# Kernel tuning notes

Hardware: AMD Instinct MI355X
Metric: run time of the kernel (lower is better)

## Reference

```python
import jax, jax.numpy as jnp
import numpy as np

B, L, DM, H = 16, 2048, 1024, 16
DK = DM // H
FACTOR = 1


def setup_inputs() -> dict:
    key = jax.random.key(0)
    ks = jax.random.split(key, 8)
    s = 0.02
    return {
        "queries": jax.random.normal(ks[0], (B, L, DM), jnp.float32),
        "keys": jax.random.normal(ks[1], (B, L, DM), jnp.float32),
        "values": jax.random.normal(ks[2], (B, L, DM), jnp.float32),
        "Wq": jax.random.normal(ks[3], (DM, DM), jnp.float32) * s,
        "Wk": jax.random.normal(ks[4], (DM, DM), jnp.float32) * s,
        "Wv": jax.random.normal(ks[5], (DM, DM), jnp.float32) * s,
        "Wo": jax.random.normal(ks[6], (DM, DM), jnp.float32) * s,
        "bo": jnp.zeros((DM,), jnp.float32),
    }


def reference(queries, keys, values, Wq, Wk, Wv, Wo, bo):
    # Projections (torch Linear: y = x @ W.T), then [B, H, DK, L] layout
    Q = (queries @ Wq.T).reshape(B, L, H, DK).transpose(0, 2, 3, 1)
    K = (keys @ Wk.T).reshape(B, L, H, DK).transpose(0, 2, 3, 1)
    V = (values @ Wv.T).reshape(B, L, H, DK).transpose(0, 2, 3, 1)

    # FFT cross-correlation along time
    qf = jnp.fft.rfft(Q, axis=-1)
    kf = jnp.fft.rfft(K, axis=-1)
    corr = jnp.fft.irfft(qf * jnp.conj(kf), n=L, axis=-1)  # [B, H, DK, L]

    # time_delay_agg_inference (eval path); B == H so torch's right-aligned
    # broadcast maps the batch axis of delay/weights onto the HEAD axis.
    top_k = int(FACTOR * np.log(L))
    mean_value = jnp.mean(corr, axis=1)                     # [B, DK, L]
    weights, delay = jax.lax.top_k(mean_value, top_k)       # [B, DK, K]
    w = jax.nn.softmax(weights, axis=-1)

    pos = jnp.arange(L)
    agg = jnp.zeros_like(V)
    for i in range(top_k):  # small fixed loop (top_k = 7)
        idx = (pos[None, None, :] + delay[:, :, i][:, :, None]) % L  # first axis aligns with H
        pattern = jnp.take_along_axis(V, jnp.broadcast_to(idx[None], V.shape), axis=-1)
        agg = agg + pattern * w[:, :, i][None, :, :, None]

    out = agg.transpose(0, 3, 1, 2).reshape(B, L, DM)  # [B, L, H*DK]
    out = out @ Wo.T + bo
    return out, corr
```

## Files before the change

kernel.cpp:

```cpp
#include <hip/hip_runtime.h>
#include <hip/hip_fp16.h>
#include <hip/hip_bf16.h>
#include <cstdint>
#include <cstddef>

typedef float  f32x4 __attribute__((ext_vector_type(4)));
typedef short  s16x8 __attribute__((ext_vector_type(8)));
typedef unsigned short u16;
typedef unsigned int   u32;
typedef u32 u32x4 __attribute__((ext_vector_type(4)));
typedef u32 u32x2 __attribute__((ext_vector_type(2)));

#define TOPK 7

__device__ __forceinline__ u32 bfpk(float re, float im) {
  __hip_bfloat162 h = __float22bfloat162_rn(make_float2(re, im));
  return *(u32*)&h;
}
__device__ __forceinline__ u16 f2bf(float f) {
  __hip_bfloat16 h = __float2bfloat16(f);
  return *(u16*)&h;
}
__device__ __forceinline__ float b2f(u16 s) {
  return __uint_as_float(((u32)s) << 16);
}
__device__ __forceinline__ float2 bfup(u32 p) {
  float2 r; r.x = b2f((u16)(p & 0xffffu)); r.y = b2f((u16)(p >> 16)); return r;
}
__device__ __forceinline__ u32 pkf16(float c, float s) {
  __half2 h = __floats2half2_rn(c, s);
  return *(u32*)&h;
}
__device__ __forceinline__ float2 upf16(u32 p) {
  __half2 h; *(u32*)&h = p;
  float2 r; r.x = __low2float(h); r.y = __high2float(h); return r;
}

typedef __attribute__((address_space(1))) void gvoid;
typedef __attribute__((address_space(3))) void lvoid;
__device__ __forceinline__ void gl_lds16(const void* g, void* l) {
  __builtin_amdgcn_global_load_lds((gvoid*)g, (lvoid*)l, 16, 0, 0);
}

__global__ void cvt_kernel(const float* __restrict__ src, u16* __restrict__ dst, int n8) {
  int i = blockIdx.x * 256 + threadIdx.x;
  if (i >= n8) return;
  const f32x4* sp = (const f32x4*)src + (size_t)i * 2;
  f32x4 a = sp[0], b = sp[1];
  u32x4 o;
  o[0] = bfpk(a[0], a[1]); o[1] = bfpk(a[2], a[3]);
  o[2] = bfpk(b[0], b[1]); o[3] = bfpk(b[2], b[3]);
  *(u32x4*)(dst + (size_t)i * 8) = o;
}

template<int MODE>
__global__ __launch_bounds__(256, 2) void gemm_bt(
    const void* __restrict__ Aptr, const u16* __restrict__ Bw,
    void* __restrict__ Cout, const float* __restrict__ bias)
{
  constexpr int K = 1024, N = 1024;
  __shared__ __align__(16) u16 lA[128 * 32];
  __shared__ __align__(16) u16 lB[128 * 32];

  int bx = blockIdx.x;
  int wg = (bx & 7) * 256 + (bx >> 3);
  int tm = wg >> 3, tn = wg & 7;
  int m0 = tm * 128, n0 = tn * 128;

  int t = threadIdx.x;
  int wid = t >> 6, lane = t & 63;
  int wm = wid >> 1, wn = wid & 1;
  int lr = lane & 15, kb = lane >> 4;

  f32x4 acc[4][4] = {};

  for (int kt = 0; kt < 32; ++kt) {
    int k0 = kt * 32;
    if constexpr (MODE == 0) {
      const float* A = (const float*)Aptr;
      int r = t >> 1, half = t & 1;
      const float* ap = A + (size_t)(m0 + r) * K + k0 + half * 16;
      f32x4 v[4];
#pragma unroll
      for (int g = 0; g < 4; ++g) v[g] = ((const f32x4*)ap)[g];
      u32x4 o0, o1;
      o0[0] = bfpk(v[0][0], v[0][1]); o0[1] = bfpk(v[0][2], v[0][3]);
      o0[2] = bfpk(v[1][0], v[1][1]); o0[3] = bfpk(v[1][2], v[1][3]);
      o1[0] = bfpk(v[2][0], v[2][1]); o1[1] = bfpk(v[2][2], v[2][3]);
      o1[2] = bfpk(v[3][0], v[3][1]); o1[3] = bfpk(v[3][2], v[3][3]);
      *(u32x4*)&lA[r * 32 + half * 16]     = o0;
      *(u32x4*)&lA[r * 32 + half * 16 + 8] = o1;
    } else {
      const u16* A = (const u16*)Aptr;
#pragma unroll
      for (int it = 0; it < 2; ++it) {
        int o = t * 16 + it * 4096;
        int e = o >> 1;
        int row = e >> 5, col = e & 31;
        gl_lds16(A + (size_t)(m0 + row) * K + k0 + col,
                 (char*)lA + wid * 1024 + it * 4096);
      }
    }
#pragma unroll
    for (int it = 0; it < 2; ++it) {
      int o = t * 16 + it * 4096;
      int e = o >> 1;
      int row = e >> 5, col = e & 31;
      gl_lds16(Bw + (size_t)(n0 + row) * K + k0 + col,
               (char*)lB + wid * 1024 + it * 4096);
    }
    __syncthreads();

    s16x8 af[4], bf[4];
#pragma unroll
    for (int mi = 0; mi < 4; ++mi)
      af[mi] = *(const s16x8*)&lA[(wm * 64 + mi * 16 + lr) * 32 + kb * 8];
#pragma unroll
    for (int ni = 0; ni < 4; ++ni)
      bf[ni] = *(const s16x8*)&lB[(wn * 64 + ni * 16 + lr) * 32 + kb * 8];
#pragma unroll
    for (int mi = 0; mi < 4; ++mi)
#pragma unroll
      for (int ni = 0; ni < 4; ++ni)
        acc[mi][ni] = __builtin_amdgcn_mfma_f32_16x16x32_bf16(af[mi], bf[ni], acc[mi][ni], 0, 0, 0);
    __syncthreads();
  }

#pragma unroll
  for (int mi = 0; mi < 4; ++mi) {
    int mbase = m0 + wm * 64 + mi * 16 + kb * 4;
#pragma unroll
    for (int ni = 0; ni < 4; ++ni) {
      int nn = n0 + wn * 64 + ni * 16 + lr;
      if constexpr (MODE == 0) {
        u16* OT = (u16*)Cout;
        int b = mbase >> 11, l = mbase & 2047;
        u32x2 pk;
        pk[0] = bfpk(acc[mi][ni][0], acc[mi][ni][1]);
        pk[1] = bfpk(acc[mi][ni][2], acc[mi][ni][3]);
        *(u32x2*)(OT + ((size_t)((b << 10) + nn)) * 2048 + l) = pk;
      } else {
        float* C = (float*)Cout;
        float bv = bias[nn];
#pragma unroll
        for (int j = 0; j < 4; ++j)
          C[(size_t)(mbase + j) * N + nn] = acc[mi][ni][j] + bv;
      }
    }
  }
}


__device__ __constant__ const int BRv[32] = {
  0,16,8,24,4,20,12,28,2,18,10,26,6,22,14,30,
  1,17,9,25,5,21,13,29,3,19,11,27,7,23,15,31};
__device__ const float C32v[16] = {
  1.0f, 0.98078528f, 0.92387953f, 0.83146961f,
  0.70710678f, 0.55557023f, 0.38268343f, 0.19509032f,
  0.0f, -0.19509032f, -0.38268343f, -0.55557023f,
  -0.70710678f, -0.83146961f, -0.92387953f, -0.98078528f};
__device__ const float S32v[16] = {
  0.0f, 0.19509032f, 0.38268343f, 0.55557023f,
  0.70710678f, 0.83146961f, 0.92387953f, 0.98078528f,
  1.0f, 0.98078528f, 0.92387953f, 0.83146961f,
  0.70710678f, 0.55557023f, 0.38268343f, 0.19509032f};

#define TWIDX(j) ((j) + ((j) >> 4))

template<bool INV>
__device__ __forceinline__ void dft32(float* xr, float* xi) {
#pragma unroll
  for (int s = 0; s < 5; ++s) {
    const int half = 1 << s, step = 16 >> s;
#pragma unroll
    for (int blk = 0; blk < 32; blk += 2 * half) {
#pragma unroll
      for (int j = 0; j < half; ++j) {
        float wr = C32v[j * step];
        float wi = INV ? S32v[j * step] : -S32v[j * step];
        int p = blk + j, q = p + half;
        float vr = xr[q] * wr - xi[q] * wi;
        float vi = xr[q] * wi + xi[q] * wr;
        xr[q] = xr[p] - vr; xi[q] = xi[p] - vi;
        xr[p] = xr[p] + vr; xi[p] = xi[p] + vi;
      }
    }
  }
}

__device__ __forceinline__ void fft_fwd_row(const u32* __restrict__ zrow, int tt,
                                            u32* wsr, const u32* twp,
                                            float* xr, float* xi) {
#pragma unroll
  for (int i = 0; i < 32; ++i) {
    float2 v = bfup(zrow[32 * BRv[i] + tt]);
    xr[i] = v.x; xi[i] = v.y;
  }
  dft32<false>(xr, xi);
#pragma unroll
  for (int k1 = 0; k1 < 32; ++k1) {
    float2 w = upf16(twp[TWIDX(tt * k1)]);
    wsr[k1 * 33 + tt] = bfpk(xr[k1] * w.x - xi[k1] * w.y,
                             xr[k1] * w.y + xi[k1] * w.x);
  }
  __syncthreads();
#pragma unroll
  for (int i = 0; i < 32; ++i) {
    float2 v = bfup(wsr[tt * 33 + BRv[i]]);
    xr[i] = v.x; xi[i] = v.y;
  }
  __syncthreads();
  dft32<false>(xr, xi);
}

__device__ __forceinline__ void spec_bin(
    float zlQr, float zlQi, float zpQr, float zpQi,
    float zlKr, float zlKi, float zpKr, float zpKi,
    float wr, float wi, float& outr, float& outi)
{
  float aQr = zlQr + zpQr, aQi = zlQi - zpQi;
  float bQr = zlQr - zpQr, bQi = zlQi + zpQi;
  float gQr  = aQr + wr * bQi + wi * bQr;
  float gQi  = aQi - (wr * bQr - wi * bQi);
  float gQpr = aQr - wr * bQi - wi * bQr;
  float gQpi = -aQi - wr * bQr + wi * bQi;
  float aKr = zlKr + zpKr, aKi = zlKi - zpKi;
  float bKr = zlKr - zpKr, bKi = zlKi + zpKi;
  float gKr  = aKr + wr * bKi + wi * bKr;
  float gKi  = aKi - (wr * bKr - wi * bKi);
  float gKpr = aKr - wr * bKi - wi * bKr;
  float gKpi = -aKi - wr * bKr + wi * bKi;
  float ctr = gQr * gKr + gQi * gKi;
  float cti = gQi * gKr - gQr * gKi;
  float cpr = gQpr * gKpr + gQpi * gKpi;
  float cpi = gQpi * gKpr - gQpr * gKpi;
  float utr = ctr + cpr, uti = cti - cpi;
  float vtr = ctr - cpr, vti = cti + cpi;
  outr = (utr - wr * vti + wi * vtr) * (1.0f / 8192.0f);
  outi = (uti + wr * vtr + wi * vti) * (1.0f / 8192.0f);
}

__global__ __launch_bounds__(256) void fftcorr_kernel(
    const u16* __restrict__ Qt, const u16* __restrict__ Kt, float* __restrict__ corr)
{
  __shared__ u32 twp[1088];
  __shared__ u32 wsb[8][1056];

  int t = threadIdx.x;
#pragma unroll
  for (int i = 0; i < 4; ++i) {
    int j = t + 256 * i;
    float s, c;
    __sincosf((float)j * -6.135923151e-3f, &s, &c);
    twp[TWIDX(j)] = pkf16(c, s);
  }
  __syncthreads();

  int rl = t >> 5, tt = t & 31;
  int row = blockIdx.x * 8 + rl;
  const u32* qrow = (const u32*)Qt + (size_t)row * 1024;
  const u32* krow = (const u32*)Kt + (size_t)row * 1024;
  u32* wsr = wsb[rl];
  int lw = t & 63;
  int paddr = (((-tt) & 31) | (lw & 32)) << 2;
  bool f0 = (tt == 0);

  float xr[32], xi[32];
  u32 zkp[32], ap[32], zcp[32];

  fft_fwd_row(krow, tt, wsr, twp, xr, xi);
#pragma unroll
  for (int i = 0; i < 32; ++i) zkp[i] = bfpk(xr[i], xi[i]);
  fft_fwd_row(qrow, tt, wsr, twp, xr, xi);
#pragma unroll
  for (int i = 0; i < 32; ++i) ap[i] = bfpk(xr[i], xi[i]);

#pragma unroll
  for (int j = 0; j < 16; ++j) {
    u32 qpA = (u32)__builtin_amdgcn_ds_bpermute(paddr, (int)ap[31 - j]);
    u32 kpA = (u32)__builtin_amdgcn_ds_bpermute(paddr, (int)zkp[31 - j]);
    u32 qpB = (u32)__builtin_amdgcn_ds_bpermute(paddr, (int)ap[j]);
    u32 kpB = (u32)__builtin_amdgcn_ds_bpermute(paddr, (int)zkp[j]);
    if (f0) {
      qpA = ap[(32 - j) & 31];  kpA = zkp[(32 - j) & 31];
      qpB = ap[(j + 1) & 31];   kpB = zkp[(j + 1) & 31];
    }
    float2 bA = upf16(twp[TWIDX((tt >> 1) + 16 * j)]);
    float2 bB = upf16(twp[TWIDX((tt >> 1) + 16 * (31 - j))]);
    bool oddk = (tt & 1);
    float mr = oddk ? 0.999995293810f : 1.0f;
    float mi = oddk ? -3.067956763e-3f : 0.0f;
    float wAr = bA.x * mr - bA.y * mi, wAi = bA.x * mi + bA.y * mr;
    float wBr = bB.x * mr - bB.y * mi, wBi = bB.x * mi + bB.y * mr;
    float2 zl, zp, kl, kp;
    float or_, oi_;
    zl = bfup(ap[j]);      zp = bfup(qpA);
    kl = bfup(zkp[j]);     kp = bfup(kpA);
    spec_bin(zl.x, zl.y, zp.x, zp.y, kl.x, kl.y, kp.x, kp.y, wAr, wAi, or_, oi_);
    zcp[j] = bfpk(or_, oi_);
    zl = bfup(ap[31 - j]); zp = bfup(qpB);
    kl = bfup(zkp[31 - j]); kp = bfup(kpB);
    spec_bin(zl.x, zl.y, zp.x, zp.y, kl.x, kl.y, kp.x, kp.y, wBr, wBi, or_, oi_);
    zcp[31 - j] = bfpk(or_, oi_);
  }

#define SWPU(a, b) { u32 tp = zcp[a]; zcp[a] = zcp[b]; zcp[b] = tp; }
  SWPU(1, 16) SWPU(2, 8) SWPU(3, 24) SWPU(5, 20) SWPU(6, 12) SWPU(7, 28)
  SWPU(9, 18) SWPU(11, 26) SWPU(13, 22) SWPU(15, 30) SWPU(19, 25) SWPU(23, 29)
#undef SWPU
#pragma unroll
  for (int i = 0; i < 32; ++i) {
    float2 v = bfup(zcp[i]);
    xr[i] = v.x; xi[i] = v.y;
  }
  dft32<true>(xr, xi);
#pragma unroll
  for (int v1 = 0; v1 < 32; ++v1) {
    float2 w = upf16(twp[TWIDX(tt * v1)]);
    wsr[v1 * 33 + tt] = bfpk(xr[v1] * w.x + xi[v1] * w.y,
                             xi[v1] * w.x - xr[v1] * w.y);
  }
  __syncthreads();
#pragma unroll
  for (int i = 0; i < 32; ++i) {
    float2 v = bfup(wsr[tt * 33 + BRv[i]]);
    xr[i] = v.x; xi[i] = v.y;
  }
  dft32<true>(xr, xi);

  float2* crow = (float2*)(corr + (size_t)row * 2048);
#pragma unroll
  for (int v2 = 0; v2 < 32; ++v2) {
    float2 o; o.x = xr[v2]; o.y = xi[v2];
    crow[tt + 32 * v2] = o;
  }
}

__global__ void mean_kernel(const float* __restrict__ corr, float* __restrict__ meanp) {
  int idx = blockIdx.x * 256 + threadIdx.x;
  int l4 = idx & 511;
  int d  = (idx >> 9) & 63;
  int b  = idx >> 15;
  const f32x4* cp = (const f32x4*)corr;
  f32x4 s = {};
#pragma unroll
  for (int h = 0; h < 16; ++h)
    s += cp[((size_t)(b * 1024 + h * 64 + d)) * 512 + l4];
  ((f32x4*)meanp)[(size_t)(b * 64 + d) * 512 + l4] = s * 0.0625f;
}

__global__ __launch_bounds__(256) void topk_kernel(
    const float* __restrict__ meanp, int* __restrict__ delays, float* __restrict__ wts)
{
  int row = blockIdx.x;
  const float* mr = meanp + (size_t)row * 2048;
  int t = threadIdx.x;
  float v[8];
#pragma unroll
  for (int j = 0; j < 8; ++j) v[j] = mr[t * 8 + j];
  __shared__ float sV[256];
  __shared__ int   sI[256];
  __shared__ float topv[TOPK];
  __shared__ int   topi[TOPK];
  for (int rnd = 0; rnd < TOPK; ++rnd) {
    float bv = v[0]; int bi = t * 8;
#pragma unroll
    for (int j = 1; j < 8; ++j)
      if (v[j] > bv) { bv = v[j]; bi = t * 8 + j; }
    sV[t] = bv; sI[t] = bi;
    __syncthreads();
    for (int off = 128; off > 0; off >>= 1) {
      if (t < off) {
        float ov = sV[t + off]; int oi = sI[t + off];
        if (ov > sV[t] || (ov == sV[t] && oi < sI[t])) { sV[t] = ov; sI[t] = oi; }
      }
      __syncthreads();
    }
    int wi = sI[0];
    if (t == 0) { topv[rnd] = sV[0]; topi[rnd] = wi; }
    if ((wi >> 3) == t) {
#pragma unroll
      for (int j = 0; j < 8; ++j)
        if ((wi & 7) == j) v[j] = -__builtin_inff();
    }
    __syncthreads();
  }
  if (t == 0) {
    float mx = topv[0], sum = 0.f, e[TOPK];
#pragma unroll
    for (int i = 0; i < TOPK; ++i) { e[i] = expf(topv[i] - mx); sum += e[i]; }
#pragma unroll
    for (int i = 0; i < TOPK; ++i) {
      wts[row * 8 + i]    = e[i] / sum;
      delays[row * 8 + i] = topi[i];
    }
  }
}

__global__ __launch_bounds__(256) void agg_kernel(
    const u16* __restrict__ Vt, const float* __restrict__ wts,
    const int* __restrict__ delays, u16* __restrict__ aggt)
{
  int row = blockIdx.x;
  int c = row & 1023;
  __shared__ __align__(16) float Vs[4608];
  __shared__ float wsh[TOPK];
  __shared__ int   dsh[TOPK];
  int t = threadIdx.x;
  if (t < TOPK) { wsh[t] = wts[c * 8 + t]; dsh[t] = delays[c * 8 + t]; }
  const u16* vr = Vt + (size_t)row * 2048;
  u32x4 rv = *(const u32x4*)(vr + t * 8);
  alignas(16) u16 uv[8];
  *(u32x4*)uv = rv;
  int f0 = t * 8;
#pragma unroll
  for (int j = 0; j < 8; ++j) {
    float fv = b2f(uv[j]);
    int f  = f0 + j;
    int f2 = f + 2048;
    Vs[f  + ((f  >> 5) << 2)] = fv;
    Vs[f2 + ((f2 >> 5) << 2)] = fv;
  }
  __syncthreads();
  float o[8] = {0, 0, 0, 0, 0, 0, 0, 0};
#pragma unroll
  for (int i = 0; i < TOPK; ++i) {
    float w = wsh[i]; int dl = dsh[i];
    int base = f0 + dl;
#pragma unroll
    for (int j = 0; j < 8; ++j) {
      int f = base + j;
      o[j] += w * Vs[f + ((f >> 5) << 2)];
    }
  }
  u32x4 ob;
  ob[0] = bfpk(o[0], o[1]); ob[1] = bfpk(o[2], o[3]);
  ob[2] = bfpk(o[4], o[5]); ob[3] = bfpk(o[6], o[7]);
  *(u32x4*)(aggt + (size_t)row * 2048 + f0) = ob;
}

__global__ __launch_bounds__(256) void transpose_kernel(
    const u16* __restrict__ aggt, u16* __restrict__ aggb)
{
  int bid = blockIdx.x;
  int lt = bid & 31;
  int ct = (bid >> 5) & 15;
  int b  = bid >> 9;
  __shared__ __align__(16) u16 tile[64][72];
  int t = threadIdx.x;
  int r = t >> 2, seg = t & 3;
  const u16* src = aggt + ((size_t)(b * 1024 + ct * 64 + r)) * 2048 + lt * 64 + seg * 16;
  u32x4 v0 = *(const u32x4*)src;
  u32x4 v1 = *(const u32x4*)(src + 8);
  *(u32x4*)&tile[r][seg * 16]     = v0;
  *(u32x4*)&tile[r][seg * 16 + 8] = v1;
  __syncthreads();
  alignas(16) u16 tmp[16];
#pragma unroll
  for (int j = 0; j < 16; ++j) tmp[j] = tile[seg * 16 + j][r];
  u16* dst = aggb + ((size_t)(b * 2048 + lt * 64 + r)) * 1024 + ct * 64 + seg * 16;
  *(u32x4*)dst       = *(u32x4*)&tmp[0];
  *(u32x4*)(dst + 8) = *(u32x4*)&tmp[8];
}

extern "C" void kernel_launch(void* const* d_in, const int* in_sizes, int n_in,
                              void* d_out, int out_size, void* d_ws, size_t ws_size,
                              hipStream_t stream) {
  (void)in_sizes; (void)n_in; (void)out_size; (void)ws_size;
  const float* qin = (const float*)d_in[0];
  const float* kin = (const float*)d_in[1];
  const float* vin = (const float*)d_in[2];
  const float* Wq  = (const float*)d_in[3];
  const float* Wk  = (const float*)d_in[4];
  const float* Wv  = (const float*)d_in[5];
  const float* Wo  = (const float*)d_in[6];
  const float* bo  = (const float*)d_in[7];

  float* out  = (float*)d_out;
  float* corr = out + (size_t)33554432;

  char* ws = (char*)d_ws;
  u16* Qt  = (u16*)ws;
  u16* Kt  = (u16*)(ws + ((size_t)64  << 20));
  u16* Vt  = (u16*)(ws + ((size_t)128 << 20));
  u16* Wqb = (u16*)(ws + ((size_t)192 << 20));
  u16* Wkb = Wqb + (1u << 20);
  u16* Wvb = Wkb + (1u << 20);
  u16* Wob = Wvb + (1u << 20);
  float* meanp  = (float*)(ws + ((size_t)200 << 20));
  int*   delays = (int*)  (ws + ((size_t)208 << 20));
  float* wts    = (float*)(ws + ((size_t)208 << 20) + 65536);
  u16* aggt = Qt;
  u16* aggb = Kt;

  dim3 blk(256);
  cvt_kernel<<<512, blk, 0, stream>>>(Wq, Wqb, 131072);
  cvt_kernel<<<512, blk, 0, stream>>>(Wk, Wkb, 131072);
  cvt_kernel<<<512, blk, 0, stream>>>(Wv, Wvb, 131072);
  cvt_kernel<<<512, blk, 0, stream>>>(Wo, Wob, 131072);

  gemm_bt<0><<<2048, blk, 0, stream>>>(qin, Wqb, Qt, nullptr);
  gemm_bt<0><<<2048, blk, 0, stream>>>(kin, Wkb, Kt, nullptr);
  gemm_bt<0><<<2048, blk, 0, stream>>>(vin, Wvb, Vt, nullptr);

  fftcorr_kernel<<<2048, blk, 0, stream>>>(Qt, Kt, corr);
  mean_kernel<<<2048, blk, 0, stream>>>(corr, meanp);
  topk_kernel<<<1024, blk, 0, stream>>>(meanp, delays, wts);
  agg_kernel<<<16384, blk, 0, stream>>>(Vt, wts, delays, aggt);
  transpose_kernel<<<8192, blk, 0, stream>>>(aggt, aggb);
  gemm_bt<1><<<2048, blk, 0, stream>>>(aggb, Wob, out, bo);
}
```

Baseline: 757.8 us.

## Double-buffer LDS tiles in projection GEMM to overlap loads with MFMA

After: 762.5 us. Within noise of the previous version (+0.6%).

```diff
diff --git a/kernel.cpp b/kernel.cpp
--- a/kernel.cpp
+++ b/kernel.cpp
@@ -59,8 +59,8 @@
     void* __restrict__ Cout, const float* __restrict__ bias)
 {
   constexpr int K = 1024, N = 1024;
-  __shared__ __align__(16) u16 lA[128 * 32];
-  __shared__ __align__(16) u16 lB[128 * 32];
+  __shared__ __align__(16) u16 lA[2][128 * 32];
+  __shared__ __align__(16) u16 lB[2][128 * 32];
 
   int bx = blockIdx.x;
   int wg = (bx & 7) * 256 + (bx >> 3);
@@ -72,58 +72,91 @@
   int wm = wid >> 1, wn = wid & 1;
   int lr = lane & 15, kb = lane >> 4;
 
+  const float* A32 = (const float*)Aptr;
+  const u16*   A16 = (const u16*)Aptr;
+  int r = t >> 1, half = t & 1;
+
   f32x4 acc[4][4] = {};
 
+  if constexpr (MODE == 0) {
+    const float* ap = A32 + (size_t)(m0 + r) * K + half * 16;
+    f32x4 v[4];
+#pragma unroll
+    for (int g = 0; g < 4; ++g) v[g] = ((const f32x4*)ap)[g];
+    u32x4 o0, o1;
+    o0[0] = bfpk(v[0][0], v[0][1]); o0[1] = bfpk(v[0][2], v[0][3]);
+    o0[2] = bfpk(v[1][0], v[1][1]); o0[3] = bfpk(v[1][2], v[1][3]);
+    o1[0] = bfpk(v[2][0], v[2][1]); o1[1] = bfpk(v[2][2], v[2][3]);
+    o1[2] = bfpk(v[3][0], v[3][1]); o1[3] = bfpk(v[3][2], v[3][3]);
+    *(u32x4*)&lA[0][r * 32 + half * 16]     = o0;
+    *(u32x4*)&lA[0][r * 32 + half * 16 + 8] = o1;
+  } else {
+#pragma unroll
+    for (int it = 0; it < 2; ++it) {
+      int e = (t * 16 + it * 4096) >> 1;
+      gl_lds16(A16 + (size_t)(m0 + (e >> 5)) * K + (e & 31),
+               (char*)&lA[0][0] + wid * 1024 + it * 4096);
+    }
+  }
+#pragma unroll
+  for (int it = 0; it < 2; ++it) {
+    int e = (t * 16 + it * 4096) >> 1;
+    gl_lds16(Bw + (size_t)(n0 + (e >> 5)) * K + (e & 31),
+             (char*)&lB[0][0] + wid * 1024 + it * 4096);
+  }
+  __syncthreads();
+
+  int cur = 0;
   for (int kt = 0; kt < 32; ++kt) {
-    int k0 = kt * 32;
-    if constexpr (MODE == 0) {
-      const float* A = (const float*)Aptr;
-      int r = t >> 1, half = t & 1;
-      const float* ap = A + (size_t)(m0 + r) * K + k0 + half * 16;
-      f32x4 v[4];
-#pragma unroll
-      for (int g = 0; g < 4; ++g) v[g] = ((const f32x4*)ap)[g];
-      u32x4 o0, o1;
-      o0[0] = bfpk(v[0][0], v[0][1]); o0[1] = bfpk(v[0][2], v[0][3]);
-      o0[2] = bfpk(v[1][0], v[1][1]); o0[3] = bfpk(v[1][2], v[1][3]);
-      o1[0] = bfpk(v[2][0], v[2][1]); o1[1] = bfpk(v[2][2], v[2][3]);
-      o1[2] = bfpk(v[3][0], v[3][1]); o1[3] = bfpk(v[3][2], v[3][3]);
-      *(u32x4*)&lA[r * 32 + half * 16]     = o0;
-      *(u32x4*)&lA[r * 32 + half * 16 + 8] = o1;
-    } else {
-      const u16* A = (const u16*)Aptr;
+    int nxt = cur ^ 1;
+    bool pf = (kt < 31);
+    f32x4 va[4];
+    if (pf) {
+      int k1 = (kt + 1) * 32;
+      if constexpr (MODE == 0) {
+        const float* ap = A32 + (size_t)(m0 + r) * K + k1 + half * 16;
+#pragma unroll
+        for (int g = 0; g < 4; ++g) va[g] = ((const f32x4*)ap)[g];
+      } else {
+#pragma unroll
+        for (int it = 0; it < 2; ++it) {
+          int e = (t * 16 + it * 4096) >> 1;
+          gl_lds16(A16 + (size_t)(m0 + (e >> 5)) * K + k1 + (e & 31),
+                   (char*)&lA[nxt][0] + wid * 1024 + it * 4096);
+        }
+      }
 #pragma unroll
       for (int it = 0; it < 2; ++it) {
-        int o = t * 16 + it * 4096;
-        int e = o >> 1;
-        int row = e >> 5, col = e & 31;
-        gl_lds16(A + (size_t)(m0 + row) * K + k0 + col,
-                 (char*)lA + wid * 1024 + it * 4096);
+        int e = (t * 16 + it * 4096) >> 1;
+        gl_lds16(Bw + (size_t)(n0 + (e >> 5)) * K + k1 + (e & 31),
+                 (char*)&lB[nxt][0] + wid * 1024 + it * 4096);
       }
     }
-#pragma unroll
-    for (int it = 0; it < 2; ++it) {
-      int o = t * 16 + it * 4096;
-      int e = o >> 1;
-      int row = e >> 5, col = e & 31;
-      gl_lds16(Bw + (size_t)(n0 + row) * K + k0 + col,
-               (char*)lB + wid * 1024 + it * 4096);
-    }
-    __syncthreads();
-
     s16x8 af[4], bf[4];
 #pragma unroll
     for (int mi = 0; mi < 4; ++mi)
-      af[mi] = *(const s16x8*)&lA[(wm * 64 + mi * 16 + lr) * 32 + kb * 8];
+      af[mi] = *(const s16x8*)&lA[cur][(wm * 64 + mi * 16 + lr) * 32 + kb * 8];
 #pragma unroll
     for (int ni = 0; ni < 4; ++ni)
-      bf[ni] = *(const s16x8*)&lB[(wn * 64 + ni * 16 + lr) * 32 + kb * 8];
+      bf[ni] = *(const s16x8*)&lB[cur][(wn * 64 + ni * 16 + lr) * 32 + kb * 8];
 #pragma unroll
     for (int mi = 0; mi < 4; ++mi)
 #pragma unroll
       for (int ni = 0; ni < 4; ++ni)
         acc[mi][ni] = __builtin_amdgcn_mfma_f32_16x16x32_bf16(af[mi], bf[ni], acc[mi][ni], 0, 0, 0);
+    if (pf) {
+      if constexpr (MODE == 0) {
+        u32x4 o0, o1;
+        o0[0] = bfpk(va[0][0], va[0][1]); o0[1] = bfpk(va[0][2], va[0][3]);
+        o0[2] = bfpk(va[1][0], va[1][1]); o0[3] = bfpk(va[1][2], va[1][3]);
+        o1[0] = bfpk(va[2][0], va[2][1]); o1[1] = bfpk(va[2][2], va[2][3]);
+        o1[2] = bfpk(va[3][0], va[3][1]); o1[3] = bfpk(va[3][2], va[3][3]);
+        *(u32x4*)&lA[nxt][r * 32 + half * 16]     = o0;
+        *(u32x4*)&lA[nxt][r * 32 + half * 16 + 8] = o1;
+      }
+    }
     __syncthreads();
+    cur = nxt;
   }
 
 #pragma unroll
```
